# Performance work log

Hardware: AMD Instinct MI355X
Metric: run time of the kernel (lower is better)

Reference implementation:

```python
import jax, jax.numpy as jnp
import numpy as np

N_NODES = 10000
N_EDGES = 320000


def _segment_softmax(scores, seg, num_segments):
    # scores: [E, H], segment-wise stable softmax keyed by seg (edge_index[0])
    m = jax.ops.segment_max(scores, seg, num_segments=num_segments)
    e = jnp.exp(scores - m[seg])
    z = jax.ops.segment_sum(e, seg, num_segments=num_segments)
    return e / z[seg]


def _gat_layer(x, W, a, row, col, n_nodes, heads, out_dim):
    # x: [N, F_in], W: [F_in, heads*out_dim], a: [heads, 2*out_dim]
    h = (x @ W).reshape(n_nodes, heads, out_dim)          # [N, H, F]
    a_l, a_r = a[:, :out_dim], a[:, out_dim:]             # [H, F] each
    # attention score per edge/head without materializing [E, H, 2F]
    s = (h[row] * a_l).sum(-1) + (h[col] * a_r).sum(-1)   # [E, H]
    alpha = _segment_softmax(s, row, n_nodes)             # [E, H]
    msg = alpha[..., None] * h[row]                       # [E, H, F]
    return jax.ops.segment_sum(msg, col, num_segments=n_nodes)  # [N, H, F]


def setup_inputs() -> dict:
    key = jax.random.key(0)
    ks = jax.random.split(key, 6)
    F, H, C = 128, 4, 22
    x = jax.random.normal(ks[0], (N_NODES, F), dtype=jnp.float32)
    edge_index = jax.random.randint(ks[1], (2, N_EDGES), 0, N_NODES, dtype=jnp.int64)
    W1 = jax.random.normal(ks[2], (F, F * H), dtype=jnp.float32) * 0.05
    a1 = jax.random.normal(ks[3], (H, 2 * F), dtype=jnp.float32) * 0.05
    W2 = jax.random.normal(ks[4], (F, C), dtype=jnp.float32) * 0.05
    a2 = jax.random.normal(ks[5], (1, 2 * C), dtype=jnp.float32) * 0.05
    return {"x": x, "edge_index": edge_index, "W1": W1, "a1": a1, "W2": W2, "a2": a2}


def reference(x, edge_index, W1, a1, W2, a2):
    row, col = edge_index[0], edge_index[1]
    h1 = _gat_layer(x, W1, a1, row, col, N_NODES, heads=4, out_dim=128)  # [N, 4, 128]
    h1 = jax.nn.elu(h1).mean(axis=1)                                      # combine heads -> [N, 128]
    h2 = _gat_layer(h1, W2, a2, row, col, N_NODES, heads=1, out_dim=22)   # [N, 1, 22]
    return h2[:, 0, :]                                                    # [N, 22]
```

## Files before the change

kernel.cpp:

```cpp
#include <hip/hip_runtime.h>

#define NN 10000
#define NE 320000
#define EPP 5000
#define NPART 64

typedef short short8 __attribute__((ext_vector_type(8)));
typedef float f32x4 __attribute__((ext_vector_type(4)));

__device__ __forceinline__ unsigned short f2bf(float f) {
    unsigned u = __float_as_uint(f);
    return (unsigned short)((u + 0x7FFFu + ((u >> 16) & 1u)) >> 16);
}
__device__ __forceinline__ float bflo(unsigned v) { return __uint_as_float(v << 16); }
__device__ __forceinline__ float bfhi(unsigned v) { return __uint_as_float(v & 0xffff0000u); }
__device__ __forceinline__ float bf1(unsigned short v) { return __uint_as_float(((unsigned)v) << 16); }

__device__ __forceinline__ int eread(const void* p, int is64, int i) {
    if (is64) return (int)((const long long*)p)[i];
    return ((const int*)p)[i];
}

__global__ __launch_bounds__(256) void k_prep0(const void* __restrict__ ei,
                                               const float* __restrict__ W1, const float* __restrict__ a1,
                                               unsigned short* __restrict__ W1t, float* __restrict__ wrf,
                                               int* __restrict__ flag) {
    const int b = blockIdx.x, t = threadIdx.x;
    if (b < 256) {
        const int g = b * 256 + t;
        const int h = g >> 14, j = (g >> 7) & 127, k = g & 127;
        W1t[g] = f2bf(W1[(size_t)k * 512 + h * 128 + j]);
    } else if (b < 258) {
        const int g = (b - 256) * 256 + t;
        const int h = g >> 7, k = g & 127;
        const float* wrow = W1 + (size_t)k * 512 + h * 128;
        const float* av = a1 + h * 256 + 128;
        float s = 0.f;
        for (int d = 0; d < 128; d++) s += wrow[d] * av[d];
        wrf[h * 128 + k] = s;
    } else {
        if (t == 0) {
            const unsigned* idx = (const unsigned*)ei;
            int all0 = 1;
            for (int j = 1; j < 257; j += 2)
                if (idx[j] != 0u) { all0 = 0; break; }
            *flag = all0;
        }
    }
}

__global__ __launch_bounds__(256) void k_pre(const float* __restrict__ x, const float* __restrict__ wrf,
                                             unsigned short* __restrict__ xb, float* __restrict__ ehr1,
                                             const void* __restrict__ ei, const int* __restrict__ flag,
                                             int* __restrict__ degp_c, int* __restrict__ degp_r,
                                             unsigned short* __restrict__ rank_c,
                                             unsigned short* __restrict__ rank_r) {
    __shared__ int sh[NN];
    const int b = blockIdx.x, t = threadIdx.x;
    if (b < 2500) {
        float* ls = (float*)sh;
        const int lane = t & 63, w = t >> 6;
        ls[t] = wrf[t];
        ls[t + 256] = wrf[t + 256];
        __syncthreads();
        const int i = b * 4 + w;
        const float x0 = x[(size_t)i * 128 + lane];
        const float x1 = x[(size_t)i * 128 + 64 + lane];
        xb[(size_t)i * 128 + lane]      = f2bf(x0);
        xb[(size_t)i * 128 + 64 + lane] = f2bf(x1);
        float v[4];
#pragma unroll
        for (int h = 0; h < 4; h++)
            v[h] = x0 * ls[h * 128 + lane] + x1 * ls[h * 128 + 64 + lane];
#pragma unroll
        for (int off = 1; off < 64; off <<= 1) {
#pragma unroll
            for (int j = 0; j < 4; j++) v[j] += __shfl_xor(v[j], off);
        }
        if (lane == 0)
            *(float4*)&ehr1[i * 4] = make_float4(__expf(v[0]), __expf(v[1]), __expf(v[2]), __expf(v[3]));
    } else {
        const int is64 = *flag;
        const int isC = (b < 2500 + NPART);
        const int p = isC ? (b - 2500) : (b - 2500 - NPART);
        const int ebase = p * EPP;
        for (int q = t; q < NN; q += 256) sh[q] = 0;
        __syncthreads();
        if (isC) {
            for (int q = t; q < EPP; q += 256) {
                const int e = ebase + q;
                const int c = eread(ei, is64, NE + e);
                rank_c[e] = (unsigned short)atomicAdd(&sh[c], 1);
            }
            __syncthreads();
            for (int q = t; q < NN; q += 256) degp_c[p * NN + q] = sh[q];
        } else {
            for (int q = t; q < EPP; q += 256) {
                const int e = ebase + q;
                const int r = eread(ei, is64, e);
                rank_r[e] = (unsigned short)atomicAdd(&sh[r], 1);
            }
            __syncthreads();
            for (int q = t; q < NN; q += 256) degp_r[p * NN + q] = sh[q];
        }
    }
}

__global__ __launch_bounds__(256) void k_psum(const int* __restrict__ degp_c, const int* __restrict__ degp_r,
                                              unsigned short* __restrict__ pfx_c, unsigned short* __restrict__ pfx_r,
                                              int* __restrict__ deg_c, int* __restrict__ deg_r) {
    const int g = blockIdx.x * 256 + threadIdx.x;
    if (g >= 2 * NN) return;
    const int arr = g / NN, node = g % NN;
    const int* degp = arr ? degp_r : degp_c;
    unsigned short* pfx = arr ? pfx_r : pfx_c;
    int* tot = arr ? deg_r : deg_c;
    int sum = 0;
    unsigned short loc[NPART];
#pragma unroll
    for (int p = 0; p < NPART; p++) {
        loc[p] = (unsigned short)sum;
        sum += degp[p * NN + node];
    }
    tot[node] = sum;
    uint4* dst = (uint4*)&pfx[(size_t)node * NPART];
#pragma unroll
    for (int q = 0; q < 8; q++)
        dst[q] = ((const uint4*)loc)[q];
}

__device__ void scan_one_1k(const int* __restrict__ deg, int* __restrict__ start, int* ssum) {
    const int t = threadIdx.x;
    int loc[10];
    const int base = t * 10;
    int sum = 0;
#pragma unroll
    for (int j = 0; j < 10; j++) {
        int i = base + j;
        int v = (i < NN) ? deg[i] : 0;
        loc[j] = sum;
        sum += v;
    }
    const int lane = t & 63, w = t >> 6;
    int xi = sum;
#pragma unroll
    for (int off = 1; off < 64; off <<= 1) {
        int y = __shfl_up(xi, off);
        if (lane >= off) xi += y;
    }
    __syncthreads();
    if (lane == 63) ssum[w] = xi;
    __syncthreads();
    int woff = 0;
#pragma unroll
    for (int k = 0; k < 16; k++)
        if (k < w) woff += ssum[k];
    const int excl = woff + xi - sum;
#pragma unroll
    for (int j = 0; j < 10; j++) {
        int i = base + j;
        if (i < NN) start[i] = excl + loc[j];
    }
}

__global__ __launch_bounds__(1024) void k_scan2(const int* __restrict__ deg_c, const int* __restrict__ deg_r,
                                                int* __restrict__ start_c, int* __restrict__ start_r) {
    __shared__ int ssum[16];
    scan_one_1k(deg_c, start_c, ssum);
    __syncthreads();
    scan_one_1k(deg_r, start_r, ssum);
}

__global__ __launch_bounds__(256) void k_build(const void* __restrict__ ei, const int* __restrict__ flag,
                                               const unsigned short* __restrict__ rank_c,
                                               const unsigned short* __restrict__ rank_r,
                                               const unsigned short* __restrict__ pfx_c,
                                               const unsigned short* __restrict__ pfx_r,
                                               const int* __restrict__ start_c, const int* __restrict__ start_r,
                                               int* __restrict__ csrA, int* __restrict__ csrB) {
    const int is64 = *flag;
    const int e = blockIdx.x * 256 + threadIdx.x;
    if (e >= NE) return;
    const int part = e / EPP;
    const int r = eread(ei, is64, e);
    const int c = eread(ei, is64, NE + e);
    csrA[start_c[c] + (int)pfx_c[(size_t)c * NPART + part] + (int)rank_c[e]] = r;
    csrB[start_r[r] + (int)pfx_r[(size_t)r * NPART + part] + (int)rank_r[e]] = c;
}

__global__ __launch_bounds__(256) void k_z1(const int* __restrict__ start_r, const int* __restrict__ deg_r,
                                            const int* __restrict__ csrB,
                                            const float* __restrict__ ehr1, float* __restrict__ rz1) {
    const int t = threadIdx.x, lane = t & 63, w = t >> 6;
    const int half = lane >> 5, l32 = lane & 31;
    const int i = blockIdx.x * 8 + w * 2 + half;
    const int s0 = start_r[i], d = deg_r[i];
    float zx = 0.f, zy = 0.f, zz = 0.f, zw = 0.f;
    for (int p = s0 + l32; p < s0 + d; p += 32) {
        const int c = csrB[p];
        const float4 v = *(const float4*)&ehr1[c * 4];
        zx += v.x; zy += v.y; zz += v.z; zw += v.w;
    }
#pragma unroll
    for (int off = 1; off < 32; off <<= 1) {
        zx += __shfl_xor(zx, off); zy += __shfl_xor(zy, off);
        zz += __shfl_xor(zz, off); zw += __shfl_xor(zw, off);
    }
    if (l32 == 0)
        *(float4*)&rz1[i * 4] = make_float4(1.f / zx, 1.f / zy, 1.f / zz, 1.f / zw);
}

__global__ __launch_bounds__(256) void k_agg1(const unsigned short* __restrict__ xb,
                                              const float* __restrict__ ehr1, const float* __restrict__ rz1,
                                              const int* __restrict__ start_c, const int* __restrict__ deg_c,
                                              const int* __restrict__ csrA,
                                              unsigned short* __restrict__ xaggb) {
    const int t = threadIdx.x, lane = t & 63, w = t >> 6;
    const int i = blockIdx.x * 4 + w;
    const float4 er4 = *(const float4*)&ehr1[i * 4];
    const int s0 = start_c[i], dg = deg_c[i];
    float acc[8];
#pragma unroll
    for (int j = 0; j < 8; j++) acc[j] = 0.f;
    int p = s0;
    const int e8 = s0 + (dg & ~7);
    for (; p < e8; p += 8) {
        int rr[8]; unsigned vv[8]; float4 zz[8];
#pragma unroll
        for (int q = 0; q < 8; q++) rr[q] = csrA[p + q];
#pragma unroll
        for (int q = 0; q < 8; q++) vv[q] = *(const unsigned*)&xb[(size_t)rr[q] * 128 + lane * 2];
#pragma unroll
        for (int q = 0; q < 8; q++) zz[q] = *(const float4*)&rz1[rr[q] * 4];
#pragma unroll
        for (int q = 0; q < 8; q++) {
            const float xa = bflo(vv[q]), xbv = bfhi(vv[q]);
            acc[0] += zz[q].x * xa; acc[1] += zz[q].x * xbv;
            acc[2] += zz[q].y * xa; acc[3] += zz[q].y * xbv;
            acc[4] += zz[q].z * xa; acc[5] += zz[q].z * xbv;
            acc[6] += zz[q].w * xa; acc[7] += zz[q].w * xbv;
        }
    }
    for (; p < s0 + dg; ++p) {
        const int r = csrA[p];
        const unsigned v = *(const unsigned*)&xb[(size_t)r * 128 + lane * 2];
        const float4 z = *(const float4*)&rz1[r * 4];
        const float xa = bflo(v), xbv = bfhi(v);
        acc[0] += z.x * xa; acc[1] += z.x * xbv;
        acc[2] += z.y * xa; acc[3] += z.y * xbv;
        acc[4] += z.z * xa; acc[5] += z.z * xbv;
        acc[6] += z.w * xa; acc[7] += z.w * xbv;
    }
    const float ef[4] = {er4.x, er4.y, er4.z, er4.w};
    unsigned short* op = xaggb + (size_t)i * 512 + lane * 2;
#pragma unroll
    for (int h = 0; h < 4; h++) {
        ushort2 st;
        st.x = f2bf(acc[h * 2] * ef[h]);
        st.y = f2bf(acc[h * 2 + 1] * ef[h]);
        *(ushort2*)(op + h * 128) = st;
    }
}

__global__ __launch_bounds__(256) void k_gemmF(const unsigned short* __restrict__ xaggb,
                                               const unsigned short* __restrict__ W1t,
                                               float* __restrict__ h1m) {
    const int t = threadIdx.x, lane = t & 63, w = t >> 6;
    const int n0 = blockIdx.x * 32;
    const int r16 = lane & 15, grp = lane >> 4;
    const int jbase = w * 32;
    f32x4 hm[2][2];
#pragma unroll
    for (int m = 0; m < 2; m++)
#pragma unroll
        for (int n = 0; n < 2; n++) hm[m][n] = (f32x4)0.f;

#pragma unroll
    for (int h = 0; h < 4; h++) {
        f32x4 acc[2][2];
#pragma unroll
        for (int m = 0; m < 2; m++)
#pragma unroll
            for (int n = 0; n < 2; n++) acc[m][n] = (f32x4)0.f;
#pragma unroll
        for (int kk = 0; kk < 128; kk += 32) {
            const int k0 = kk + grp * 8;
            short8 a0 = *(const short8*)&xaggb[((size_t)(n0 + r16) * 4 + h) * 128 + k0];
            short8 a1 = *(const short8*)&xaggb[((size_t)(n0 + 16 + r16) * 4 + h) * 128 + k0];
            short8 b0 = *(const short8*)&W1t[(size_t)h * 16384 + (jbase + r16) * 128 + k0];
            short8 b1 = *(const short8*)&W1t[(size_t)h * 16384 + (jbase + 16 + r16) * 128 + k0];
            acc[0][0] = __builtin_amdgcn_mfma_f32_16x16x32_bf16(a0, b0, acc[0][0], 0, 0, 0);
            acc[1][0] = __builtin_amdgcn_mfma_f32_16x16x32_bf16(a1, b0, acc[1][0], 0, 0, 0);
            acc[0][1] = __builtin_amdgcn_mfma_f32_16x16x32_bf16(a0, b1, acc[0][1], 0, 0, 0);
            acc[1][1] = __builtin_amdgcn_mfma_f32_16x16x32_bf16(a1, b1, acc[1][1], 0, 0, 0);
        }
#pragma unroll
        for (int m = 0; m < 2; m++)
#pragma unroll
            for (int n = 0; n < 2; n++)
#pragma unroll
                for (int r = 0; r < 4; r++) {
                    const float v = acc[m][n][r];
                    hm[m][n][r] += (v > 0.f) ? v : (__expf(v) - 1.f);
                }
    }
#pragma unroll
    for (int m = 0; m < 2; m++)
#pragma unroll
        for (int n = 0; n < 2; n++)
#pragma unroll
            for (int r = 0; r < 4; r++) {
                const int node = n0 + m * 16 + grp * 4 + r;
                const int col = jbase + n * 16 + r16;
                h1m[(size_t)node * 128 + col] = 0.25f * hm[m][n][r];
            }
}

__global__ __launch_bounds__(256) void k_gemm2(const float* __restrict__ h1m, const float* __restrict__ W2,
                                               const float* __restrict__ a2,
                                               float* __restrict__ h2, float* __restrict__ ehr2) {
    __shared__ float sh[4][128];
    const int t = threadIdx.x, lane = t & 63, w = t >> 6;
    const int i = blockIdx.x * 4 + w;
    sh[w][lane]      = h1m[(size_t)i * 128 + lane];
    sh[w][lane + 64] = h1m[(size_t)i * 128 + 64 + lane];
    __syncthreads();
    const int seg = lane >> 5, c = lane & 31;
    float part = 0.f;
    if (c < 22) {
        const int kb = seg * 64;
        for (int k = kb; k < kb + 64; k++)
            part += sh[w][k] * W2[k * 22 + c];
    }
    part += __shfl_xor(part, 32);
    const float acc = part;
    if (lane < 22) h2[(size_t)i * 22 + lane] = acc;
    float pr = (lane < 22) ? acc * a2[22 + lane] : 0.f;
#pragma unroll
    for (int off = 1; off < 64; off <<= 1)
        pr += __shfl_xor(pr, off);
    if (lane == 0) ehr2[i] = __expf(pr);
}

__global__ __launch_bounds__(256) void k_z2s(const int* __restrict__ start_r, const int* __restrict__ deg_r,
                                             const int* __restrict__ csrB,
                                             const float* __restrict__ ehr2, const float* __restrict__ h2,
                                             unsigned short* __restrict__ h2s) {
    const int t = threadIdx.x, lane = t & 63, w = t >> 6;
    const int half = lane >> 5, l32 = lane & 31;
    const int i = blockIdx.x * 8 + w * 2 + half;
    const int s0 = start_r[i], d = deg_r[i];
    float z = 0.f;
    for (int p = s0 + l32; p < s0 + d; p += 32)
        z += ehr2[csrB[p]];
#pragma unroll
    for (int off = 1; off < 32; off <<= 1)
        z += __shfl_xor(z, off);
    const float rz = 1.f / z;
    if (l32 < 22)
        h2s[(size_t)i * 22 + l32] = f2bf(h2[(size_t)i * 22 + l32] * rz);
}

__global__ __launch_bounds__(256) void k_agg2(const unsigned short* __restrict__ h2s,
                                              const float* __restrict__ ehr2,
                                              const int* __restrict__ start_c, const int* __restrict__ deg_c,
                                              const int* __restrict__ csrA,
                                              float* __restrict__ out) {
    const int t = threadIdx.x, lane = t & 63, w = t >> 6;
    const int half = lane >> 5, c32 = lane & 31;
    const int i = blockIdx.x * 8 + w * 2 + half;
    const int s0 = start_c[i], dg = deg_c[i];
    const float e2 = ehr2[i];
    const int c = (c32 < 22) ? c32 : 0;
    float acc = 0.f;
    int p = s0;
    const int e4 = s0 + (dg & ~3);
    for (; p < e4; p += 4) {
        const int r0 = csrA[p], r1 = csrA[p + 1], r2 = csrA[p + 2], r3 = csrA[p + 3];
        const float v0 = bf1(h2s[(size_t)r0 * 22 + c]);
        const float v1 = bf1(h2s[(size_t)r1 * 22 + c]);
        const float v2 = bf1(h2s[(size_t)r2 * 22 + c]);
        const float v3 = bf1(h2s[(size_t)r3 * 22 + c]);
        acc += v0 + v1 + v2 + v3;
    }
    for (; p < s0 + dg; ++p) {
        const int r = csrA[p];
        acc += bf1(h2s[(size_t)r * 22 + c]);
    }
    if (c32 < 22) out[(size_t)i * 22 + c32] = acc * e2;
}

extern "C" void kernel_launch(void* const* d_in, const int* in_sizes, int n_in,
                              void* d_out, int out_size, void* d_ws, size_t ws_size,
                              hipStream_t stream) {
    const float* x  = (const float*)d_in[0];
    const void*  ei = d_in[1];
    const float* W1 = (const float*)d_in[2];
    const float* a1 = (const float*)d_in[3];
    const float* W2 = (const float*)d_in[4];
    const float* a2 = (const float*)d_in[5];
    float* out = (float*)d_out;

    float* ws = (float*)d_ws;
    unsigned short* xaggb = (unsigned short*)ws;
    float* h1m  = ws + 2600000;
    float* h2   = ws + 3890000;
    float* ehr1 = ws + 4110000;
    float* rz1  = ws + 4150000;
    float* ehr2 = ws + 4190000;
    unsigned short* h2s = (unsigned short*)(ws + 4200000);
    int* deg_c   = (int*)(ws + 4310000);
    int* deg_r   = (int*)(ws + 4320000);
    int* start_c = (int*)(ws + 4330000);
    int* start_r = (int*)(ws + 4340000);
    int* csrA    = (int*)(ws + 4350000);
    int* csrB    = (int*)(ws + 4670000);
    int* flag    = (int*)(ws + 4990000);
    float* wrf   = ws + 4990064;
    unsigned short* W1t = (unsigned short*)(ws + 4991000);
    unsigned short* xb  = (unsigned short*)(ws + 5024000);
    unsigned short* rank_c = (unsigned short*)(ws + 5664000);
    unsigned short* rank_r = (unsigned short*)(ws + 5824000);
    int* degp_c = (int*)(ws + 5984000);
    int* degp_r = (int*)(ws + 6624000);
    unsigned short* pfx_c = (unsigned short*)(ws + 7264000);
    unsigned short* pfx_r = (unsigned short*)(ws + 7584000);

    k_prep0<<<259, 256, 0, stream>>>(ei, W1, a1, W1t, wrf, flag);
    k_pre<<<2500 + 2 * NPART, 256, 0, stream>>>(x, wrf, xb, ehr1, ei, flag,
                                                degp_c, degp_r, rank_c, rank_r);
    k_psum<<<79, 256, 0, stream>>>(degp_c, degp_r, pfx_c, pfx_r, deg_c, deg_r);
    k_scan2<<<1, 1024, 0, stream>>>(deg_c, deg_r, start_c, start_r);
    k_build<<<1250, 256, 0, stream>>>(ei, flag, rank_c, rank_r, pfx_c, pfx_r,
                                      start_c, start_r, csrA, csrB);
    k_z1<<<1250, 256, 0, stream>>>(start_r, deg_r, csrB, ehr1, rz1);
    k_agg1<<<2500, 256, 0, stream>>>(xb, ehr1, rz1, start_c, deg_c, csrA, xaggb);
    k_gemmF<<<313, 256, 0, stream>>>(xaggb, W1t, h1m);
    k_gemm2<<<2500, 256, 0, stream>>>(h1m, W2, a2, h2, ehr2);
    k_z2s<<<1250, 256, 0, stream>>>(start_r, deg_r, csrB, ehr2, h2, h2s);
    k_agg2<<<1250, 256, 0, stream>>>(h2s, ehr2, start_c, deg_c, csrA, out);
}
```

Baseline: 116.4 us.

## Pack node id with rank, narrow partial degrees, transpose prefix layout, pad h2s rows

The degree-count pass now stores each edge's node id and local rank packed in one 32-bit word. The CSR build therefore no longer re-reads the (possibly 64-bit) edge_index or needs the format flag. Per-partition degree counts shrink to 16 bits, and the prefix table is transposed to [part][node], so both the psum writes and the build lookups are coalesced. The layer-2 scaled features are padded to a 32-element row stride, and the aggregation loop unrolls by 8 for more loads in flight. These changes add workspace layout shifts and assume node ids fit in 19 bits and ranks in 13 bits.

Measured after the change: 112.3 us. -3.5%, faster.

```diff
diff --git a/kernel.cpp b/kernel.cpp
--- a/kernel.cpp
+++ b/kernel.cpp
@@ -52,9 +52,10 @@
 __global__ __launch_bounds__(256) void k_pre(const float* __restrict__ x, const float* __restrict__ wrf,
                                              unsigned short* __restrict__ xb, float* __restrict__ ehr1,
                                              const void* __restrict__ ei, const int* __restrict__ flag,
-                                             int* __restrict__ degp_c, int* __restrict__ degp_r,
-                                             unsigned short* __restrict__ rank_c,
-                                             unsigned short* __restrict__ rank_r) {
+                                             unsigned short* __restrict__ degp_c,
+                                             unsigned short* __restrict__ degp_r,
+                                             unsigned* __restrict__ packed_c,
+                                             unsigned* __restrict__ packed_r) {
     __shared__ int sh[NN];
     const int b = blockIdx.x, t = threadIdx.x;
     if (b < 2500) {
@@ -90,43 +91,42 @@
             for (int q = t; q < EPP; q += 256) {
                 const int e = ebase + q;
                 const int c = eread(ei, is64, NE + e);
-                rank_c[e] = (unsigned short)atomicAdd(&sh[c], 1);
+                const unsigned rk = (unsigned)atomicAdd(&sh[c], 1);
+                packed_c[e] = ((unsigned)c << 13) | rk;
             }
             __syncthreads();
-            for (int q = t; q < NN; q += 256) degp_c[p * NN + q] = sh[q];
+            for (int q = t; q < NN; q += 256) degp_c[p * NN + q] = (unsigned short)sh[q];
         } else {
             for (int q = t; q < EPP; q += 256) {
                 const int e = ebase + q;
                 const int r = eread(ei, is64, e);
-                rank_r[e] = (unsigned short)atomicAdd(&sh[r], 1);
+                const unsigned rk = (unsigned)atomicAdd(&sh[r], 1);
+                packed_r[e] = ((unsigned)r << 13) | rk;
             }
             __syncthreads();
-            for (int q = t; q < NN; q += 256) degp_r[p * NN + q] = sh[q];
+            for (int q = t; q < NN; q += 256) degp_r[p * NN + q] = (unsigned short)sh[q];
         }
     }
 }
 
-__global__ __launch_bounds__(256) void k_psum(const int* __restrict__ degp_c, const int* __restrict__ degp_r,
-                                              unsigned short* __restrict__ pfx_c, unsigned short* __restrict__ pfx_r,
+__global__ __launch_bounds__(256) void k_psum(const unsigned short* __restrict__ degp_c,
+                                              const unsigned short* __restrict__ degp_r,
+                                              unsigned short* __restrict__ pfx_c,
+                                              unsigned short* __restrict__ pfx_r,
                                               int* __restrict__ deg_c, int* __restrict__ deg_r) {
     const int g = blockIdx.x * 256 + threadIdx.x;
     if (g >= 2 * NN) return;
     const int arr = g / NN, node = g % NN;
-    const int* degp = arr ? degp_r : degp_c;
+    const unsigned short* degp = arr ? degp_r : degp_c;
     unsigned short* pfx = arr ? pfx_r : pfx_c;
     int* tot = arr ? deg_r : deg_c;
     int sum = 0;
-    unsigned short loc[NPART];
 #pragma unroll
     for (int p = 0; p < NPART; p++) {
-        loc[p] = (unsigned short)sum;
-        sum += degp[p * NN + node];
+        pfx[p * NN + node] = (unsigned short)sum;
+        sum += (int)degp[p * NN + node];
     }
     tot[node] = sum;
-    uint4* dst = (uint4*)&pfx[(size_t)node * NPART];
-#pragma unroll
-    for (int q = 0; q < 8; q++)
-        dst[q] = ((const uint4*)loc)[q];
 }
 
 __device__ void scan_one_1k(const int* __restrict__ deg, int* __restrict__ start, int* ssum) {
@@ -171,21 +171,20 @@
     scan_one_1k(deg_r, start_r, ssum);
 }
 
-__global__ __launch_bounds__(256) void k_build(const void* __restrict__ ei, const int* __restrict__ flag,
-                                               const unsigned short* __restrict__ rank_c,
-                                               const unsigned short* __restrict__ rank_r,
+__global__ __launch_bounds__(256) void k_build(const unsigned* __restrict__ packed_c,
+                                               const unsigned* __restrict__ packed_r,
                                                const unsigned short* __restrict__ pfx_c,
                                                const unsigned short* __restrict__ pfx_r,
                                                const int* __restrict__ start_c, const int* __restrict__ start_r,
                                                int* __restrict__ csrA, int* __restrict__ csrB) {
-    const int is64 = *flag;
     const int e = blockIdx.x * 256 + threadIdx.x;
     if (e >= NE) return;
     const int part = e / EPP;
-    const int r = eread(ei, is64, e);
-    const int c = eread(ei, is64, NE + e);
-    csrA[start_c[c] + (int)pfx_c[(size_t)c * NPART + part] + (int)rank_c[e]] = r;
-    csrB[start_r[r] + (int)pfx_r[(size_t)r * NPART + part] + (int)rank_r[e]] = c;
+    const unsigned pc = packed_c[e], pr = packed_r[e];
+    const int c = (int)(pc >> 13), rkc = (int)(pc & 8191u);
+    const int r = (int)(pr >> 13), rkr = (int)(pr & 8191u);
+    csrA[start_c[c] + (int)pfx_c[part * NN + c] + rkc] = r;
+    csrB[start_r[r] + (int)pfx_r[part * NN + r] + rkr] = c;
 }
 
 __global__ __launch_bounds__(256) void k_z1(const int* __restrict__ start_r, const int* __restrict__ deg_r,
@@ -358,7 +357,7 @@
         z += __shfl_xor(z, off);
     const float rz = 1.f / z;
     if (l32 < 22)
-        h2s[(size_t)i * 22 + l32] = f2bf(h2[(size_t)i * 22 + l32] * rz);
+        h2s[(size_t)i * 32 + l32] = f2bf(h2[(size_t)i * 22 + l32] * rz);
 }
 
 __global__ __launch_bounds__(256) void k_agg2(const unsigned short* __restrict__ h2s,
@@ -374,18 +373,20 @@
     const int c = (c32 < 22) ? c32 : 0;
     float acc = 0.f;
     int p = s0;
-    const int e4 = s0 + (dg & ~3);
-    for (; p < e4; p += 4) {
-        const int r0 = csrA[p], r1 = csrA[p + 1], r2 = csrA[p + 2], r3 = csrA[p + 3];
-        const float v0 = bf1(h2s[(size_t)r0 * 22 + c]);
-        const float v1 = bf1(h2s[(size_t)r1 * 22 + c]);
-        const float v2 = bf1(h2s[(size_t)r2 * 22 + c]);
-        const float v3 = bf1(h2s[(size_t)r3 * 22 + c]);
-        acc += v0 + v1 + v2 + v3;
+    const int e8 = s0 + (dg & ~7);
+    for (; p < e8; p += 8) {
+        int rr[8];
+#pragma unroll
+        for (int q = 0; q < 8; q++) rr[q] = csrA[p + q];
+        float vv[8];
+#pragma unroll
+        for (int q = 0; q < 8; q++) vv[q] = bf1(h2s[(size_t)rr[q] * 32 + c]);
+#pragma unroll
+        for (int q = 0; q < 8; q++) acc += vv[q];
     }
     for (; p < s0 + dg; ++p) {
         const int r = csrA[p];
-        acc += bf1(h2s[(size_t)r * 22 + c]);
+        acc += bf1(h2s[(size_t)r * 32 + c]);
     }
     if (c32 < 22) out[(size_t)i * 22 + c32] = acc * e2;
 }
@@ -409,29 +410,29 @@
     float* rz1  = ws + 4150000;
     float* ehr2 = ws + 4190000;
     unsigned short* h2s = (unsigned short*)(ws + 4200000);
-    int* deg_c   = (int*)(ws + 4310000);
-    int* deg_r   = (int*)(ws + 4320000);
-    int* start_c = (int*)(ws + 4330000);
-    int* start_r = (int*)(ws + 4340000);
-    int* csrA    = (int*)(ws + 4350000);
-    int* csrB    = (int*)(ws + 4670000);
-    int* flag    = (int*)(ws + 4990000);
-    float* wrf   = ws + 4990064;
-    unsigned short* W1t = (unsigned short*)(ws + 4991000);
-    unsigned short* xb  = (unsigned short*)(ws + 5024000);
-    unsigned short* rank_c = (unsigned short*)(ws + 5664000);
-    unsigned short* rank_r = (unsigned short*)(ws + 5824000);
-    int* degp_c = (int*)(ws + 5984000);
-    int* degp_r = (int*)(ws + 6624000);
-    unsigned short* pfx_c = (unsigned short*)(ws + 7264000);
-    unsigned short* pfx_r = (unsigned short*)(ws + 7584000);
+    int* deg_c   = (int*)(ws + 4360000);
+    int* deg_r   = (int*)(ws + 4370000);
+    int* start_c = (int*)(ws + 4380000);
+    int* start_r = (int*)(ws + 4390000);
+    int* csrA    = (int*)(ws + 4400000);
+    int* csrB    = (int*)(ws + 4720000);
+    int* flag    = (int*)(ws + 5040000);
+    float* wrf   = ws + 5040064;
+    unsigned short* W1t = (unsigned short*)(ws + 5041000);
+    unsigned short* xb  = (unsigned short*)(ws + 5074000);
+    unsigned* packed_c = (unsigned*)(ws + 5714000);
+    unsigned* packed_r = (unsigned*)(ws + 6034000);
+    unsigned short* degp_c = (unsigned short*)(ws + 6354000);
+    unsigned short* degp_r = (unsigned short*)(ws + 6674000);
+    unsigned short* pfx_c  = (unsigned short*)(ws + 6994000);
+    unsigned short* pfx_r  = (unsigned short*)(ws + 7314000);
 
     k_prep0<<<259, 256, 0, stream>>>(ei, W1, a1, W1t, wrf, flag);
     k_pre<<<2500 + 2 * NPART, 256, 0, stream>>>(x, wrf, xb, ehr1, ei, flag,
-                                                degp_c, degp_r, rank_c, rank_r);
+                                                degp_c, degp_r, packed_c, packed_r);
     k_psum<<<79, 256, 0, stream>>>(degp_c, degp_r, pfx_c, pfx_r, deg_c, deg_r);
     k_scan2<<<1, 1024, 0, stream>>>(deg_c, deg_r, start_c, start_r);
-    k_build<<<1250, 256, 0, stream>>>(ei, flag, rank_c, rank_r, pfx_c, pfx_r,
+    k_build<<<1250, 256, 0, stream>>>(packed_c, packed_r, pfx_c, pfx_r,
                                       start_c, start_r, csrA, csrB);
     k_z1<<<1250, 256, 0, stream>>>(start_r, deg_r, csrB, ehr1, rz1);
     k_agg1<<<2500, 256, 0, stream>>>(xb, ehr1, rz1, start_c, deg_c, csrA, xaggb);
```
